# Kernel tuning notes

Hardware: AMD Instinct MI355X
Metric: run time of the kernel (lower is better)

The kernel has to match this reference:

```python
import jax, jax.numpy as jnp
import numpy as np

N = 50000       # nodes
E = 1600000     # edges (before self-loops)
IN = 128        # in_channels
HID = 64        # hidden_channels
HEADS = 2
OUT = 16        # out_channels
NEG_SLOPE = 0.2 # PyG GATConv default leaky_relu slope


def setup_inputs() -> dict:
    key = jax.random.key(0)
    ks = jax.random.split(key, 12)
    g = lambda k, shp, s=0.1: (jax.random.normal(k, shp, dtype=jnp.float32) * s)
    return {
        "x": jax.random.normal(ks[0], (N, IN), dtype=jnp.float32),
        "edge_index": jax.random.randint(ks[1], (2, E), 0, N, dtype=jnp.int32),
        # layer 0: in -> hidden, heads concat
        "W0": g(ks[2], (IN, HEADS * HID)),
        "as0": g(ks[3], (HEADS, HID)),
        "ad0": g(ks[4], (HEADS, HID)),
        "b0": jnp.zeros((HEADS * HID,), jnp.float32),
        # layer 1: hidden*heads -> hidden, heads concat
        "W1": g(ks[5], (HEADS * HID, HEADS * HID)),
        "as1": g(ks[6], (HEADS, HID)),
        "ad1": g(ks[7], (HEADS, HID)),
        "b1": jnp.zeros((HEADS * HID,), jnp.float32),
        # layer 2: hidden*heads -> out, heads averaged (concat=False)
        "W2": g(ks[8], (HEADS * HID, HEADS * OUT)),
        "as2": g(ks[9], (HEADS, OUT)),
        "ad2": g(ks[10], (HEADS, OUT)),
        "b2": jnp.zeros((OUT,), jnp.float32),
    }


def gat_conv(x, src, dst, W, a_src, a_dst, b, concat):
    """PyG-style GATConv (inference; self-loops already in src/dst)."""
    n = x.shape[0]
    H, C = a_src.shape
    h = (x @ W).reshape(n, H, C)                      # [N,H,C]
    alpha_s = jnp.einsum('nhc,hc->nh', h, a_src)      # [N,H]
    alpha_d = jnp.einsum('nhc,hc->nh', h, a_dst)      # [N,H]
    e = alpha_s[src] + alpha_d[dst]                   # [E,H]
    e = jax.nn.leaky_relu(e, NEG_SLOPE)
    # softmax over incoming edges per destination node
    m = jax.ops.segment_max(e, dst, num_segments=n)   # [N,H]
    w = jnp.exp(e - m[dst])                           # [E,H]
    denom = jax.ops.segment_sum(w, dst, num_segments=n)
    alpha = w / (denom[dst] + 1e-16)                  # [E,H]
    out = jax.ops.segment_sum(alpha[:, :, None] * h[src], dst, num_segments=n)  # [N,H,C]
    out = out.reshape(n, H * C) if concat else out.mean(axis=1)
    return out + b


def reference(x, edge_index, W0, as0, ad0, b0, W1, as1, ad1, b1, W2, as2, ad2, b2):
    loop = jnp.arange(N, dtype=edge_index.dtype)
    src = jnp.concatenate([edge_index[0], loop])
    dst = jnp.concatenate([edge_index[1], loop])
    h = jax.nn.elu(gat_conv(x, src, dst, W0, as0, ad0, b0, concat=True))
    h = jax.nn.elu(gat_conv(h, src, dst, W1, as1, ad1, b1, concat=True))
    return gat_conv(h, src, dst, W2, as2, ad2, b2, concat=False)
```

## Files before the change

### kernel.cpp

```cpp
#include <hip/hip_runtime.h>
#include <hip/hip_fp16.h>
#include <cstdint>
#include <cstddef>
#include <type_traits>

constexpr int kN   = 50000;
constexpr int kE   = 1600000;
constexpr int kET  = kE + kN;
constexpr float kNEG = 0.2f;
constexpr int NBUCK = (kN + 127) / 128;
constexpr int CAPB  = 5120;
constexpr int PCHUNK = 4096;
constexpr int PGRID = (kET + PCHUNK - 1) / PCHUNK;

__global__ __launch_bounds__(256) void partition_kernel(const int* __restrict__ ei,
                                                        int* __restrict__ bcnt,
                                                        unsigned* __restrict__ part) {
  __shared__ int hist[NBUCK];
  __shared__ int resv[NBUCK];
  __shared__ int lcnt[NBUCK];
  const int t = threadIdx.x;
  for (int i = t; i < NBUCK; i += 256) hist[i] = 0;
  __syncthreads();
  const int c0 = blockIdx.x * PCHUNK;
  const int cend = (c0 + PCHUNK < kET) ? c0 + PCHUNK : kET;
  for (int i = c0 + t; i < cend; i += 256) {
    const int dst = (i < kE) ? ei[kE + i] : (i - kE);
    atomicAdd(&hist[dst >> 7], 1);
  }
  __syncthreads();
  for (int i = t; i < NBUCK; i += 256) {
    lcnt[i] = 0;
    if (hist[i]) resv[i] = i * CAPB + atomicAdd(&bcnt[i], hist[i]);
  }
  __syncthreads();
  for (int i = c0 + t; i < cend; i += 256) {
    int src, dst;
    if (i < kE) { src = ei[i]; dst = ei[kE + i]; }
    else        { src = i - kE; dst = src; }
    const int b = dst >> 7;
    const int off = atomicAdd(&lcnt[b], 1);
    part[resv[b] + off] = ((unsigned)(dst & 127) << 16) | (unsigned)src;
  }
}

__global__ __launch_bounds__(256) void finalize_kernel(const unsigned* __restrict__ part,
                                                       const int* __restrict__ bcnt,
                                                       int* __restrict__ row_beg,
                                                       int* __restrict__ row_cnt,
                                                       int* __restrict__ col_src) {
  __shared__ int cnt[128];
  __shared__ int sc[128];
  __shared__ int nbase[128];
  const int b = blockIdx.x, t = threadIdx.x;
  const int lo = b * CAPB;
  const int hi = lo + bcnt[b];
  if (t < 128) cnt[t] = 0;
  __syncthreads();
  for (int j = lo + t; j < hi; j += 256) atomicAdd(&cnt[part[j] >> 16], 1);
  __syncthreads();
  if (t < 128) sc[t] = cnt[t];
  __syncthreads();
  for (int off = 1; off < 128; off <<= 1) {
    int v = 0;
    if (t < 128 && t >= off) v = sc[t - off];
    __syncthreads();
    if (t < 128) sc[t] += v;
    __syncthreads();
  }
  if (t < 128) {
    const int c = cnt[t];
    nbase[t] = lo + sc[t] - c;
    const int node = b * 128 + t;
    if (node < kN) { row_beg[node] = nbase[t]; row_cnt[node] = c; }
    cnt[t] = 0;
  }
  __syncthreads();
  for (int j = lo + t; j < hi; j += 256) {
    const unsigned v = part[j];
    const int nl = v >> 16;
    const int pos = nbase[nl] + atomicAdd(&cnt[nl], 1);
    col_src[pos] = (int)(v & 0xffffu);
  }
}

template<int MOUT, int TR, typename TIN>
__global__ __launch_bounds__(256) void transform_kernel(
    const TIN* __restrict__ X, const float* __restrict__ W,
    const float* __restrict__ asf, const float* __restrict__ adf,
    __half* __restrict__ H2, float2* __restrict__ AS, float2* __restrict__ AD, int n) {
  constexpr int CG = MOUT / 4;
  constexpr int RG = 256 / CG;
  constexpr int ROWS = RG * TR;
  __shared__ float Xs[ROWS][132];
  const int t = threadIdx.x;
  const int row0 = blockIdx.x * ROWS;
  if constexpr (std::is_same<TIN, float>::value) {
    for (int i = t; i < ROWS * 32; i += 256) {
      const int r = i >> 5, kc = i & 31;
      float4 v = make_float4(0.f, 0.f, 0.f, 0.f);
      if (row0 + r < n) v = ((const float4*)(X + (size_t)(row0 + r) * 128))[kc];
      *(float4*)(&Xs[r][kc * 4]) = v;
    }
  } else {
    for (int i = t; i < ROWS * 16; i += 256) {
      const int r = i >> 4, kc = i & 15;
      union { uint4 u; __half2 h[4]; } raw;
      raw.u = make_uint4(0u, 0u, 0u, 0u);
      if (row0 + r < n) raw.u = *(const uint4*)(X + (size_t)(row0 + r) * 128 + kc * 8);
      const float2 f0 = __half22float2(raw.h[0]);
      const float2 f1 = __half22float2(raw.h[1]);
      const float2 f2 = __half22float2(raw.h[2]);
      const float2 f3 = __half22float2(raw.h[3]);
      *(float4*)(&Xs[r][kc * 8])     = make_float4(f0.x, f0.y, f1.x, f1.y);
      *(float4*)(&Xs[r][kc * 8 + 4]) = make_float4(f2.x, f2.y, f3.x, f3.y);
    }
  }
  __syncthreads();
  const int cg = t % CG;
  const int rg = t / CG;
  const int c0 = cg * 4;
  float4 acc[TR];
#pragma unroll
  for (int i = 0; i < TR; i++) acc[i] = make_float4(0.f, 0.f, 0.f, 0.f);
  for (int k4 = 0; k4 < 32; k4++) {
    float4 wv0 = *(const float4*)(W + (size_t)(k4 * 4 + 0) * MOUT + c0);
    float4 wv1 = *(const float4*)(W + (size_t)(k4 * 4 + 1) * MOUT + c0);
    float4 wv2 = *(const float4*)(W + (size_t)(k4 * 4 + 2) * MOUT + c0);
    float4 wv3 = *(const float4*)(W + (size_t)(k4 * 4 + 3) * MOUT + c0);
#pragma unroll
    for (int i = 0; i < TR; i++) {
      const float4 xv = *(const float4*)(&Xs[rg * TR + i][k4 * 4]);
      acc[i].x = fmaf(xv.x, wv0.x, acc[i].x); acc[i].y = fmaf(xv.x, wv0.y, acc[i].y);
      acc[i].z = fmaf(xv.x, wv0.z, acc[i].z); acc[i].w = fmaf(xv.x, wv0.w, acc[i].w);
      acc[i].x = fmaf(xv.y, wv1.x, acc[i].x); acc[i].y = fmaf(xv.y, wv1.y, acc[i].y);
      acc[i].z = fmaf(xv.y, wv1.z, acc[i].z); acc[i].w = fmaf(xv.y, wv1.w, acc[i].w);
      acc[i].x = fmaf(xv.z, wv2.x, acc[i].x); acc[i].y = fmaf(xv.z, wv2.y, acc[i].y);
      acc[i].z = fmaf(xv.z, wv2.z, acc[i].z); acc[i].w = fmaf(xv.z, wv2.w, acc[i].w);
      acc[i].x = fmaf(xv.w, wv3.x, acc[i].x); acc[i].y = fmaf(xv.w, wv3.y, acc[i].y);
      acc[i].z = fmaf(xv.w, wv3.z, acc[i].z); acc[i].w = fmaf(xv.w, wv3.w, acc[i].w);
    }
  }
#pragma unroll
  for (int i = 0; i < TR; i++) {
    const int r = row0 + rg * TR + i;
    if (r < n) {
      union { __half2 h[2]; uint2 u; } pk;
      pk.h[0] = __floats2half2_rn(acc[i].x, acc[i].y);
      pk.h[1] = __floats2half2_rn(acc[i].z, acc[i].w);
      *(uint2*)(H2 + (size_t)r * MOUT + c0) = pk.u;
    }
  }
  const float4 av = *(const float4*)(asf + c0);
  const float4 dv = *(const float4*)(adf + c0);
  float sred[TR], dred[TR];
#pragma unroll
  for (int i = 0; i < TR; i++) {
    sred[i] = acc[i].x * av.x + acc[i].y * av.y + acc[i].z * av.z + acc[i].w * av.w;
    dred[i] = acc[i].x * dv.x + acc[i].y * dv.y + acc[i].z * dv.z + acc[i].w * dv.w;
  }
#pragma unroll
  for (int off = 1; off < CG / 2; off <<= 1) {
#pragma unroll
    for (int i = 0; i < TR; i++) {
      sred[i] += __shfl_xor(sred[i], off);
      dred[i] += __shfl_xor(dred[i], off);
    }
  }
  const int lane = t & 63;
#pragma unroll
  for (int i = 0; i < TR; i++) {
    const float s1 = __shfl(sred[i], lane + CG / 2);
    const float d1 = __shfl(dred[i], lane + CG / 2);
    if (cg == 0) {
      const int r = row0 + rg * TR + i;
      if (r < n) { AS[r] = make_float2(sred[i], s1); AD[r] = make_float2(dred[i], d1); }
    }
  }
}

template<int C, int MODE, typename TOUT>
__global__ __launch_bounds__(256) void agg_kernel(
    const __half* __restrict__ H2, const float2* __restrict__ AS,
    const float2* __restrict__ AD, const int* __restrict__ row_beg,
    const int* __restrict__ row_cnt, const int* __restrict__ col_src,
    const float* __restrict__ bias, TOUT* __restrict__ OUT) {
  const int wid  = threadIdx.x >> 6;
  const int lane = threadIdx.x & 63;
  const int node = blockIdx.x * 4 + wid;

  const int begin = row_beg[node];
  const int d = row_cnt[node];
  const float2 adn = AD[node];

  int srcv = 0;
  unsigned pkw = 0;
  float sum0 = 0.f, sum1 = 0.f;
  if (lane < d) {
    srcv = col_src[begin + lane];
    const float2 a = AS[srcv];
    float e0 = a.x + adn.x; e0 = (e0 > 0.f) ? e0 : kNEG * e0;
    float e1 = a.y + adn.y; e1 = (e1 > 0.f) ? e1 : kNEG * e1;
    sum0 = __expf(e0); sum1 = __expf(e1);
    const __half2 ph = __floats2half2_rn(sum0, sum1);
    pkw = *(const unsigned*)&ph;
  }
  for (int j = 64 + lane; j < d; j += 64) {
    const int s = col_src[begin + j];
    const float2 a = AS[s];
    float e0 = a.x + adn.x; e0 = (e0 > 0.f) ? e0 : kNEG * e0;
    float e1 = a.y + adn.y; e1 = (e1 > 0.f) ? e1 : kNEG * e1;
    sum0 += __expf(e0); sum1 += __expf(e1);
  }
#pragma unroll
  for (int off = 32; off >= 1; off >>= 1) {
    sum0 += __shfl_xor(sum0, off);
    sum1 += __shfl_xor(sum1, off);
  }
  const float inv0 = 1.0f / (sum0 + 1e-16f);
  const float inv1 = 1.0f / (sum1 + 1e-16f);

  const int dr = (d < 64) ? d : 64;

  if constexpr (MODE == 0) {
    const int e = lane >> 4;
    const int q = lane & 15;
    const int hsel = (q >= 8);
    const unsigned sel = hsel ? 0x03020302u : 0x01000100u;
    const float inv = hsel ? inv1 : inv0;
    float4 a0 = make_float4(0.f, 0.f, 0.f, 0.f);
    float4 a1 = make_float4(0.f, 0.f, 0.f, 0.f);
    int j = 0;
    while (j < dr) {
      const int jend = (j + 32 < dr) ? j + 32 : dr;
      __half2 hz; *(unsigned*)&hz = 0u;
      __half2 hc0 = hz, hc1 = hz, hc2 = hz, hc3 = hz;
      for (; j < jend; j += 4) {
        const int jj = j + e;
        const int s = __shfl(srcv, jj);
        const unsigned pw = __shfl((int)pkw, jj);
        union { unsigned u; __half2 h; } wv;
        wv.u = __builtin_amdgcn_perm(pw, pw, sel);
        union { uint4 u; __half2 h[4]; } raw;
        raw.u = *(const uint4*)(H2 + (size_t)s * 128 + 8 * q);
        hc0 = __hfma2(wv.h, raw.h[0], hc0);
        hc1 = __hfma2(wv.h, raw.h[1], hc1);
        hc2 = __hfma2(wv.h, raw.h[2], hc2);
        hc3 = __hfma2(wv.h, raw.h[3], hc3);
      }
      float2 f;
      f = __half22float2(hc0); a0.x += f.x; a0.y += f.y;
      f = __half22float2(hc1); a0.z += f.x; a0.w += f.y;
      f = __half22float2(hc2); a1.x += f.x; a1.y += f.y;
      f = __half22float2(hc3); a1.z += f.x; a1.w += f.y;
    }
    for (int jt = 64 + e; jt < d; jt += 4) {
      const int s = col_src[begin + jt];
      const float2 a = AS[s];
      float e0 = a.x + adn.x; e0 = (e0 > 0.f) ? e0 : kNEG * e0;
      float e1 = a.y + adn.y; e1 = (e1 > 0.f) ? e1 : kNEG * e1;
      const float w = hsel ? __expf(e1) : __expf(e0);
      union { uint4 u; __half2 h[4]; } raw;
      raw.u = *(const uint4*)(H2 + (size_t)s * 128 + 8 * q);
      const float2 f0 = __half22float2(raw.h[0]);
      const float2 f1 = __half22float2(raw.h[1]);
      const float2 f2 = __half22float2(raw.h[2]);
      const float2 f3 = __half22float2(raw.h[3]);
      a0.x = fmaf(w, f0.x, a0.x); a0.y = fmaf(w, f0.y, a0.y);
      a0.z = fmaf(w, f1.x, a0.z); a0.w = fmaf(w, f1.y, a0.w);
      a1.x = fmaf(w, f2.x, a1.x); a1.y = fmaf(w, f2.y, a1.y);
      a1.z = fmaf(w, f3.x, a1.z); a1.w = fmaf(w, f3.y, a1.w);
    }
#pragma unroll
    for (int off = 32; off >= 16; off >>= 1) {
      a0.x += __shfl_xor(a0.x, off); a0.y += __shfl_xor(a0.y, off);
      a0.z += __shfl_xor(a0.z, off); a0.w += __shfl_xor(a0.w, off);
      a1.x += __shfl_xor(a1.x, off); a1.y += __shfl_xor(a1.y, off);
      a1.z += __shfl_xor(a1.z, off); a1.w += __shfl_xor(a1.w, off);
    }
    if (lane < 16) {
      const int ch = 8 * q;
      const float4 b0v = *(const float4*)(bias + ch);
      const float4 b1v = *(const float4*)(bias + ch + 4);
      float4 o0, o1;
      o0.x = a0.x * inv + b0v.x; o0.y = a0.y * inv + b0v.y;
      o0.z = a0.z * inv + b0v.z; o0.w = a0.w * inv + b0v.w;
      o1.x = a1.x * inv + b1v.x; o1.y = a1.y * inv + b1v.y;
      o1.z = a1.z * inv + b1v.z; o1.w = a1.w * inv + b1v.w;
      o0.x = (o0.x > 0.f) ? o0.x : expm1f(o0.x);
      o0.y = (o0.y > 0.f) ? o0.y : expm1f(o0.y);
      o0.z = (o0.z > 0.f) ? o0.z : expm1f(o0.z);
      o0.w = (o0.w > 0.f) ? o0.w : expm1f(o0.w);
      o1.x = (o1.x > 0.f) ? o1.x : expm1f(o1.x);
      o1.y = (o1.y > 0.f) ? o1.y : expm1f(o1.y);
      o1.z = (o1.z > 0.f) ? o1.z : expm1f(o1.z);
      o1.w = (o1.w > 0.f) ? o1.w : expm1f(o1.w);
      if constexpr (std::is_same<TOUT, __half>::value) {
        union { __half2 h[4]; uint4 u; } pk;
        pk.h[0] = __floats2half2_rn(o0.x, o0.y);
        pk.h[1] = __floats2half2_rn(o0.z, o0.w);
        pk.h[2] = __floats2half2_rn(o1.x, o1.y);
        pk.h[3] = __floats2half2_rn(o1.z, o1.w);
        *(uint4*)(OUT + (size_t)node * 128 + ch) = pk.u;
      } else {
        *(float4*)((float*)OUT + (size_t)node * 128 + ch) = o0;
        *(float4*)((float*)OUT + (size_t)node * 128 + ch + 4) = o1;
      }
    }
  } else {
    const int e = lane >> 3;
    const int q = lane & 7;
    const int hsel = (q >= 4);
    const unsigned sel = hsel ? 0x03020302u : 0x01000100u;
    const float inv = hsel ? inv1 : inv0;
    __half2 hz; *(unsigned*)&hz = 0u;
    __half2 hc0 = hz, hc1 = hz;
    for (int j = 0; j < dr; j += 8) {
      const int jj = j + e;
      const int s = __shfl(srcv, jj);
      const unsigned pw = __shfl((int)pkw, jj);
      union { unsigned u; __half2 h; } wv;
      wv.u = __builtin_amdgcn_perm(pw, pw, sel);
      union { uint2 u; __half2 h[2]; } raw;
      raw.u = *(const uint2*)(H2 + (size_t)s * 32 + 4 * q);
      hc0 = __hfma2(wv.h, raw.h[0], hc0);
      hc1 = __hfma2(wv.h, raw.h[1], hc1);
    }
    float4 acc;
    float2 f;
    f = __half22float2(hc0); acc.x = f.x; acc.y = f.y;
    f = __half22float2(hc1); acc.z = f.x; acc.w = f.y;
    for (int jt = 64 + e; jt < d; jt += 8) {
      const int s = col_src[begin + jt];
      const float2 a = AS[s];
      float e0 = a.x + adn.x; e0 = (e0 > 0.f) ? e0 : kNEG * e0;
      float e1 = a.y + adn.y; e1 = (e1 > 0.f) ? e1 : kNEG * e1;
      const float w = hsel ? __expf(e1) : __expf(e0);
      union { uint2 u; __half2 h[2]; } raw;
      raw.u = *(const uint2*)(H2 + (size_t)s * 32 + 4 * q);
      const float2 f0 = __half22float2(raw.h[0]);
      const float2 f1 = __half22float2(raw.h[1]);
      acc.x = fmaf(w, f0.x, acc.x); acc.y = fmaf(w, f0.y, acc.y);
      acc.z = fmaf(w, f1.x, acc.z); acc.w = fmaf(w, f1.y, acc.w);
    }
#pragma unroll
    for (int off = 32; off >= 8; off >>= 1) {
      acc.x += __shfl_xor(acc.x, off); acc.y += __shfl_xor(acc.y, off);
      acc.z += __shfl_xor(acc.z, off); acc.w += __shfl_xor(acc.w, off);
    }
    acc.x *= inv; acc.y *= inv; acc.z *= inv; acc.w *= inv;
    const float px = __shfl_xor(acc.x, 4);
    const float py = __shfl_xor(acc.y, 4);
    const float pz = __shfl_xor(acc.z, 4);
    const float pw = __shfl_xor(acc.w, 4);
    if (lane < 4) {
      const int ch = 4 * q;
      const float4 bv = *(const float4*)(bias + ch);
      float4 o;
      o.x = 0.5f * (acc.x + px) + bv.x;
      o.y = 0.5f * (acc.y + py) + bv.y;
      o.z = 0.5f * (acc.z + pz) + bv.z;
      o.w = 0.5f * (acc.w + pw) + bv.w;
      *(float4*)((float*)OUT + (size_t)node * 16 + ch) = o;
    }
  }
}

extern "C" void kernel_launch(void* const* d_in, const int* in_sizes, int n_in,
                              void* d_out, int out_size, void* d_ws, size_t ws_size,
                              hipStream_t stream) {
  const float* x   = (const float*)d_in[0];
  const int*   ei  = (const int*)d_in[1];
  const float* W0  = (const float*)d_in[2];
  const float* as0 = (const float*)d_in[3];
  const float* ad0 = (const float*)d_in[4];
  const float* b0  = (const float*)d_in[5];
  const float* W1  = (const float*)d_in[6];
  const float* as1 = (const float*)d_in[7];
  const float* ad1 = (const float*)d_in[8];
  const float* b1  = (const float*)d_in[9];
  const float* W2  = (const float*)d_in[10];
  const float* as2 = (const float*)d_in[11];
  const float* ad2 = (const float*)d_in[12];
  const float* b2  = (const float*)d_in[13];
  float* out = (float*)d_out;

  size_t off = 0;
  auto alloc = [&](size_t bytes) -> void* {
    void* p = (char*)d_ws + off;
    off += (bytes + 255) & ~(size_t)255;
    return p;
  };
  int*    row_beg = (int*)alloc(sizeof(int) * kN);
  int*    row_cnt = (int*)alloc(sizeof(int) * kN);
  int*    bcnt    = (int*)alloc(sizeof(int) * NBUCK);
  int*    col_src = (int*)alloc(sizeof(int) * (size_t)NBUCK * CAPB);
  float2* AS      = (float2*)alloc(sizeof(float2) * kN);
  float2* AD      = (float2*)alloc(sizeof(float2) * kN);
  __half* H2      = (__half*)alloc(sizeof(__half) * (size_t)kN * 128);
  __half* actA    = (__half*)alloc(sizeof(__half) * (size_t)kN * 128);
  __half* actB    = (__half*)alloc(sizeof(__half) * (size_t)kN * 128);
  unsigned* part  = (unsigned*)actA;
  (void)ws_size; (void)in_sizes; (void)n_in; (void)out_size;

  hipMemsetAsync(bcnt, 0, sizeof(int) * NBUCK, stream);
  partition_kernel<<<PGRID, 256, 0, stream>>>(ei, bcnt, part);
  finalize_kernel<<<NBUCK, 256, 0, stream>>>(part, bcnt, row_beg, row_cnt, col_src);

  transform_kernel<128, 4, float><<<(kN + 31) / 32, 256, 0, stream>>>(x, W0, as0, ad0, H2, AS, AD, kN);
  agg_kernel<64, 0, __half><<<(kN + 3) / 4, 256, 0, stream>>>(H2, AS, AD, row_beg, row_cnt, col_src, b0, actA);

  transform_kernel<128, 4, __half><<<(kN + 31) / 32, 256, 0, stream>>>(actA, W1, as1, ad1, H2, AS, AD, kN);
  agg_kernel<64, 0, __half><<<(kN + 3) / 4, 256, 0, stream>>>(H2, AS, AD, row_beg, row_cnt, col_src, b1, actB);

  transform_kernel<32, 1, __half><<<(kN + 31) / 32, 256, 0, stream>>>(actB, W2, as2, ad2, H2, AS, AD, kN);
  agg_kernel<16, 1, float><<<(kN + 3) / 4, 256, 0, stream>>>(H2, AS, AD, row_beg, row_cnt, col_src, b2, out);
}
```

Measured before the change: 300.7 us.

## Split attention weights into separate pass and quarter-partition aggregation by channel

```diff
diff --git a/kernel.cpp b/kernel.cpp
--- a/kernel.cpp
+++ b/kernel.cpp
@@ -12,6 +12,7 @@
 constexpr int CAPB  = 5120;
 constexpr int PCHUNK = 4096;
 constexpr int PGRID = (kET + PCHUNK - 1) / PCHUNK;
+constexpr int QSTRIDE = kN * 32;
 
 __global__ __launch_bounds__(256) void partition_kernel(const int* __restrict__ ei,
                                                         int* __restrict__ bcnt,
@@ -148,7 +149,13 @@
       union { __half2 h[2]; uint2 u; } pk;
       pk.h[0] = __floats2half2_rn(acc[i].x, acc[i].y);
       pk.h[1] = __floats2half2_rn(acc[i].z, acc[i].w);
-      *(uint2*)(H2 + (size_t)r * MOUT + c0) = pk.u;
+      if constexpr (MOUT == 128) {
+        const int qq = cg >> 3;
+        const int co = (cg & 7) * 4;
+        *(uint2*)(H2 + (size_t)qq * QSTRIDE + (size_t)r * 32 + co) = pk.u;
+      } else {
+        *(uint2*)(H2 + (size_t)r * MOUT + c0) = pk.u;
+      }
     }
   }
   const float4 av = *(const float4*)(asf + c0);
@@ -179,32 +186,28 @@
   }
 }
 
-template<int C, int MODE, typename TOUT>
-__global__ __launch_bounds__(256) void agg_kernel(
-    const __half* __restrict__ H2, const float2* __restrict__ AS,
-    const float2* __restrict__ AD, const int* __restrict__ row_beg,
-    const int* __restrict__ row_cnt, const int* __restrict__ col_src,
-    const float* __restrict__ bias, TOUT* __restrict__ OUT) {
+__global__ __launch_bounds__(256) void weight_kernel(
+    const float2* __restrict__ AS, const float2* __restrict__ AD,
+    const int* __restrict__ row_beg, const int* __restrict__ row_cnt,
+    const int* __restrict__ col_src,
+    unsigned* __restrict__ rec0, unsigned* __restrict__ rec1) {
   const int wid  = threadIdx.x >> 6;
   const int lane = threadIdx.x & 63;
   const int node = blockIdx.x * 4 + wid;
-
   const int begin = row_beg[node];
   const int d = row_cnt[node];
   const float2 adn = AD[node];
 
   int srcv = 0;
-  unsigned pkw = 0;
-  float sum0 = 0.f, sum1 = 0.f;
+  float w0 = 0.f, w1 = 0.f;
   if (lane < d) {
     srcv = col_src[begin + lane];
     const float2 a = AS[srcv];
     float e0 = a.x + adn.x; e0 = (e0 > 0.f) ? e0 : kNEG * e0;
     float e1 = a.y + adn.y; e1 = (e1 > 0.f) ? e1 : kNEG * e1;
-    sum0 = __expf(e0); sum1 = __expf(e1);
-    const __half2 ph = __floats2half2_rn(sum0, sum1);
-    pkw = *(const unsigned*)&ph;
-  }
+    w0 = __expf(e0); w1 = __expf(e1);
+  }
+  float sum0 = w0, sum1 = w1;
   for (int j = 64 + lane; j < d; j += 64) {
     const int s = col_src[begin + j];
     const float2 a = AS[s];
@@ -219,150 +222,154 @@
   }
   const float inv0 = 1.0f / (sum0 + 1e-16f);
   const float inv1 = 1.0f / (sum1 + 1e-16f);
-
-  const int dr = (d < 64) ? d : 64;
-
-  if constexpr (MODE == 0) {
-    const int e = lane >> 4;
-    const int q = lane & 15;
-    const int hsel = (q >= 8);
-    const unsigned sel = hsel ? 0x03020302u : 0x01000100u;
-    const float inv = hsel ? inv1 : inv0;
-    float4 a0 = make_float4(0.f, 0.f, 0.f, 0.f);
-    float4 a1 = make_float4(0.f, 0.f, 0.f, 0.f);
-    int j = 0;
-    while (j < dr) {
-      const int jend = (j + 32 < dr) ? j + 32 : dr;
-      __half2 hz; *(unsigned*)&hz = 0u;
-      __half2 hc0 = hz, hc1 = hz, hc2 = hz, hc3 = hz;
-      for (; j < jend; j += 4) {
-        const int jj = j + e;
-        const int s = __shfl(srcv, jj);
-        const unsigned pw = __shfl((int)pkw, jj);
-        union { unsigned u; __half2 h; } wv;
-        wv.u = __builtin_amdgcn_perm(pw, pw, sel);
-        union { uint4 u; __half2 h[4]; } raw;
-        raw.u = *(const uint4*)(H2 + (size_t)s * 128 + 8 * q);
-        hc0 = __hfma2(wv.h, raw.h[0], hc0);
-        hc1 = __hfma2(wv.h, raw.h[1], hc1);
-        hc2 = __hfma2(wv.h, raw.h[2], hc2);
-        hc3 = __hfma2(wv.h, raw.h[3], hc3);
-      }
-      float2 f;
-      f = __half22float2(hc0); a0.x += f.x; a0.y += f.y;
-      f = __half22float2(hc1); a0.z += f.x; a0.w += f.y;
-      f = __half22float2(hc2); a1.x += f.x; a1.y += f.y;
-      f = __half22float2(hc3); a1.z += f.x; a1.w += f.y;
-    }
-    for (int jt = 64 + e; jt < d; jt += 4) {
-      const int s = col_src[begin + jt];
-      const float2 a = AS[s];
-      float e0 = a.x + adn.x; e0 = (e0 > 0.f) ? e0 : kNEG * e0;
-      float e1 = a.y + adn.y; e1 = (e1 > 0.f) ? e1 : kNEG * e1;
-      const float w = hsel ? __expf(e1) : __expf(e0);
+  if (lane < d) {
+    const unsigned h0 = (unsigned)__half_as_ushort(__float2half_rn(w0 * inv0));
+    const unsigned h1 = (unsigned)__half_as_ushort(__float2half_rn(w1 * inv1));
+    rec0[begin + lane] = (unsigned)srcv | (h0 << 16);
+    rec1[begin + lane] = (unsigned)srcv | (h1 << 16);
+  }
+  for (int j = 64 + lane; j < d; j += 64) {
+    const int s = col_src[begin + j];
+    const float2 a = AS[s];
+    float e0 = a.x + adn.x; e0 = (e0 > 0.f) ? e0 : kNEG * e0;
+    float e1 = a.y + adn.y; e1 = (e1 > 0.f) ? e1 : kNEG * e1;
+    const unsigned h0 = (unsigned)__half_as_ushort(__float2half_rn(__expf(e0) * inv0));
+    const unsigned h1 = (unsigned)__half_as_ushort(__float2half_rn(__expf(e1) * inv1));
+    rec0[begin + j] = (unsigned)s | (h0 << 16);
+    rec1[begin + j] = (unsigned)s | (h1 << 16);
+  }
+}
+
+__global__ __launch_bounds__(256) void agg64q_kernel(
+    const __half* __restrict__ H2q, const unsigned* __restrict__ rec0,
+    const unsigned* __restrict__ rec1, const int* __restrict__ row_beg,
+    const int* __restrict__ row_cnt, const float* __restrict__ bias,
+    __half* __restrict__ OUT) {
+  const int bid = blockIdx.x;
+  const int qtr = (bid & 7) >> 1;
+  const int ng  = ((bid >> 3) << 1) | (bid & 1);
+  const int wid  = threadIdx.x >> 6;
+  const int lane = threadIdx.x & 63;
+  const int node = ng * 4 + wid;
+  const int begin = row_beg[node];
+  const int d = row_cnt[node];
+  const unsigned* __restrict__ rec = (qtr >= 2) ? rec1 : rec0;
+  const int strm = lane >> 2;
+  const int cq   = lane & 3;
+  const __half* __restrict__ Hq = H2q + (size_t)qtr * QSTRIDE;
+
+  float4 f0 = make_float4(0.f, 0.f, 0.f, 0.f);
+  float4 f1 = make_float4(0.f, 0.f, 0.f, 0.f);
+  int j = 0;
+  while (j < d) {
+    const int jend = (j + 64 < d) ? j + 64 : d;
+    __half2 hz; *(unsigned*)&hz = 0u;
+    __half2 hc0 = hz, hc1 = hz, hc2 = hz, hc3 = hz;
+    for (; j < jend; j += 16) {
+      const int jo = j + strm;
+      const int jc = (jo < d) ? jo : 0;
+      unsigned r = rec[begin + jc];
+      if (jo >= d) r &= 0xffffu;
+      union { unsigned u; __half2 h; } wv;
+      wv.u = __builtin_amdgcn_perm(r, r, 0x03020302u);
       union { uint4 u; __half2 h[4]; } raw;
-      raw.u = *(const uint4*)(H2 + (size_t)s * 128 + 8 * q);
-      const float2 f0 = __half22float2(raw.h[0]);
-      const float2 f1 = __half22float2(raw.h[1]);
-      const float2 f2 = __half22float2(raw.h[2]);
-      const float2 f3 = __half22float2(raw.h[3]);
-      a0.x = fmaf(w, f0.x, a0.x); a0.y = fmaf(w, f0.y, a0.y);
-      a0.z = fmaf(w, f1.x, a0.z); a0.w = fmaf(w, f1.y, a0.w);
-      a1.x = fmaf(w, f2.x, a1.x); a1.y = fmaf(w, f2.y, a1.y);
-      a1.z = fmaf(w, f3.x, a1.z); a1.w = fmaf(w, f3.y, a1.w);
-    }
-#pragma unroll
-    for (int off = 32; off >= 16; off >>= 1) {
-      a0.x += __shfl_xor(a0.x, off); a0.y += __shfl_xor(a0.y, off);
-      a0.z += __shfl_xor(a0.z, off); a0.w += __shfl_xor(a0.w, off);
-      a1.x += __shfl_xor(a1.x, off); a1.y += __shfl_xor(a1.y, off);
-      a1.z += __shfl_xor(a1.z, off); a1.w += __shfl_xor(a1.w, off);
-    }
-    if (lane < 16) {
-      const int ch = 8 * q;
-      const float4 b0v = *(const float4*)(bias + ch);
-      const float4 b1v = *(const float4*)(bias + ch + 4);
-      float4 o0, o1;
-      o0.x = a0.x * inv + b0v.x; o0.y = a0.y * inv + b0v.y;
-      o0.z = a0.z * inv + b0v.z; o0.w = a0.w * inv + b0v.w;
-      o1.x = a1.x * inv + b1v.x; o1.y = a1.y * inv + b1v.y;
-      o1.z = a1.z * inv + b1v.z; o1.w = a1.w * inv + b1v.w;
-      o0.x = (o0.x > 0.f) ? o0.x : expm1f(o0.x);
-      o0.y = (o0.y > 0.f) ? o0.y : expm1f(o0.y);
-      o0.z = (o0.z > 0.f) ? o0.z : expm1f(o0.z);
-      o0.w = (o0.w > 0.f) ? o0.w : expm1f(o0.w);
-      o1.x = (o1.x > 0.f) ? o1.x : expm1f(o1.x);
-      o1.y = (o1.y > 0.f) ? o1.y : expm1f(o1.y);
-      o1.z = (o1.z > 0.f) ? o1.z : expm1f(o1.z);
-      o1.w = (o1.w > 0.f) ? o1.w : expm1f(o1.w);
-      if constexpr (std::is_same<TOUT, __half>::value) {
-        union { __half2 h[4]; uint4 u; } pk;
-        pk.h[0] = __floats2half2_rn(o0.x, o0.y);
-        pk.h[1] = __floats2half2_rn(o0.z, o0.w);
-        pk.h[2] = __floats2half2_rn(o1.x, o1.y);
-        pk.h[3] = __floats2half2_rn(o1.z, o1.w);
-        *(uint4*)(OUT + (size_t)node * 128 + ch) = pk.u;
-      } else {
-        *(float4*)((float*)OUT + (size_t)node * 128 + ch) = o0;
-        *(float4*)((float*)OUT + (size_t)node * 128 + ch + 4) = o1;
-      }
-    }
-  } else {
-    const int e = lane >> 3;
-    const int q = lane & 7;
-    const int hsel = (q >= 4);
-    const unsigned sel = hsel ? 0x03020302u : 0x01000100u;
-    const float inv = hsel ? inv1 : inv0;
+      raw.u = *(const uint4*)(Hq + (size_t)(r & 0xffffu) * 32 + (cq << 3));
+      hc0 = __hfma2(wv.h, raw.h[0], hc0);
+      hc1 = __hfma2(wv.h, raw.h[1], hc1);
+      hc2 = __hfma2(wv.h, raw.h[2], hc2);
+      hc3 = __hfma2(wv.h, raw.h[3], hc3);
+    }
+    float2 f;
+    f = __half22float2(hc0); f0.x += f.x; f0.y += f.y;
+    f = __half22float2(hc1); f0.z += f.x; f0.w += f.y;
+    f = __half22float2(hc2); f1.x += f.x; f1.y += f.y;
+    f = __half22float2(hc3); f1.z += f.x; f1.w += f.y;
+  }
+#pragma unroll
+  for (int off = 32; off >= 4; off >>= 1) {
+    f0.x += __shfl_xor(f0.x, off); f0.y += __shfl_xor(f0.y, off);
+    f0.z += __shfl_xor(f0.z, off); f0.w += __shfl_xor(f0.w, off);
+    f1.x += __shfl_xor(f1.x, off); f1.y += __shfl_xor(f1.y, off);
+    f1.z += __shfl_xor(f1.z, off); f1.w += __shfl_xor(f1.w, off);
+  }
+  if (lane < 4) {
+    const int ch = qtr * 32 + lane * 8;
+    const float4 b0v = *(const float4*)(bias + ch);
+    const float4 b1v = *(const float4*)(bias + ch + 4);
+    float4 o0, o1;
+    o0.x = f0.x + b0v.x; o0.y = f0.y + b0v.y; o0.z = f0.z + b0v.z; o0.w = f0.w + b0v.w;
+    o1.x = f1.x + b1v.x; o1.y = f1.y + b1v.y; o1.z = f1.z + b1v.z; o1.w = f1.w + b1v.w;
+    o0.x = (o0.x > 0.f) ? o0.x : expm1f(o0.x);
+    o0.y = (o0.y > 0.f) ? o0.y : expm1f(o0.y);
+    o0.z = (o0.z > 0.f) ? o0.z : expm1f(o0.z);
+    o0.w = (o0.w > 0.f) ? o0.w : expm1f(o0.w);
+    o1.x = (o1.x > 0.f) ? o1.x : expm1f(o1.x);
+    o1.y = (o1.y > 0.f) ? o1.y : expm1f(o1.y);
+    o1.z = (o1.z > 0.f) ? o1.z : expm1f(o1.z);
+    o1.w = (o1.w > 0.f) ? o1.w : expm1f(o1.w);
+    union { __half2 h[4]; uint4 u; } pk;
+    pk.h[0] = __floats2half2_rn(o0.x, o0.y);
+    pk.h[1] = __floats2half2_rn(o0.z, o0.w);
+    pk.h[2] = __floats2half2_rn(o1.x, o1.y);
+    pk.h[3] = __floats2half2_rn(o1.z, o1.w);
+    *(uint4*)(OUT + (size_t)node * 128 + ch) = pk.u;
+  }
+}
+
+__global__ __launch_bounds__(256) void agg16r_kernel(
+    const __half* __restrict__ H2, const unsigned* __restrict__ rec0,
+    const unsigned* __restrict__ rec1, const int* __restrict__ row_beg,
+    const int* __restrict__ row_cnt, const float* __restrict__ bias,
+    float* __restrict__ OUT) {
+  const int wid  = threadIdx.x >> 6;
+  const int lane = threadIdx.x & 63;
+  const int node = blockIdx.x * 4 + wid;
+  const int begin = row_beg[node];
+  const int d = row_cnt[node];
+  const int strm = lane >> 3;
+  const int q    = lane & 7;
+  const unsigned* __restrict__ rec = (q >= 4) ? rec1 : rec0;
+
+  float4 acc = make_float4(0.f, 0.f, 0.f, 0.f);
+  int j = 0;
+  while (j < d) {
+    const int jend = (j + 64 < d) ? j + 64 : d;
     __half2 hz; *(unsigned*)&hz = 0u;
     __half2 hc0 = hz, hc1 = hz;
-    for (int j = 0; j < dr; j += 8) {
-      const int jj = j + e;
-      const int s = __shfl(srcv, jj);
-      const unsigned pw = __shfl((int)pkw, jj);
+    for (; j < jend; j += 8) {
+      const int jo = j + strm;
+      const int jc = (jo < d) ? jo : 0;
+      unsigned r = rec[begin + jc];
+      if (jo >= d) r &= 0xffffu;
       union { unsigned u; __half2 h; } wv;
-      wv.u = __builtin_amdgcn_perm(pw, pw, sel);
+      wv.u = __builtin_amdgcn_perm(r, r, 0x03020302u);
       union { uint2 u; __half2 h[2]; } raw;
-      raw.u = *(const uint2*)(H2 + (size_t)s * 32 + 4 * q);
+      raw.u = *(const uint2*)(H2 + (size_t)(r & 0xffffu) * 32 + (q << 2));
       hc0 = __hfma2(wv.h, raw.h[0], hc0);
       hc1 = __hfma2(wv.h, raw.h[1], hc1);
     }
-    float4 acc;
     float2 f;
-    f = __half22float2(hc0); acc.x = f.x; acc.y = f.y;
-    f = __half22float2(hc1); acc.z = f.x; acc.w = f.y;
-    for (int jt = 64 + e; jt < d; jt += 8) {
-      const int s = col_src[begin + jt];
-      const float2 a = AS[s];
-      float e0 = a.x + adn.x; e0 = (e0 > 0.f) ? e0 : kNEG * e0;
-      float e1 = a.y + adn.y; e1 = (e1 > 0.f) ? e1 : kNEG * e1;
-      const float w = hsel ? __expf(e1) : __expf(e0);
-      union { uint2 u; __half2 h[2]; } raw;
-      raw.u = *(const uint2*)(H2 + (size_t)s * 32 + 4 * q);
-      const float2 f0 = __half22float2(raw.h[0]);
-      const float2 f1 = __half22float2(raw.h[1]);
-      acc.x = fmaf(w, f0.x, acc.x); acc.y = fmaf(w, f0.y, acc.y);
-      acc.z = fmaf(w, f1.x, acc.z); acc.w = fmaf(w, f1.y, acc.w);
-    }
-#pragma unroll
-    for (int off = 32; off >= 8; off >>= 1) {
-      acc.x += __shfl_xor(acc.x, off); acc.y += __shfl_xor(acc.y, off);
-      acc.z += __shfl_xor(acc.z, off); acc.w += __shfl_xor(acc.w, off);
-    }
-    acc.x *= inv; acc.y *= inv; acc.z *= inv; acc.w *= inv;
-    const float px = __shfl_xor(acc.x, 4);
-    const float py = __shfl_xor(acc.y, 4);
-    const float pz = __shfl_xor(acc.z, 4);
-    const float pw = __shfl_xor(acc.w, 4);
-    if (lane < 4) {
-      const int ch = 4 * q;
-      const float4 bv = *(const float4*)(bias + ch);
-      float4 o;
-      o.x = 0.5f * (acc.x + px) + bv.x;
-      o.y = 0.5f * (acc.y + py) + bv.y;
-      o.z = 0.5f * (acc.z + pz) + bv.z;
-      o.w = 0.5f * (acc.w + pw) + bv.w;
-      *(float4*)((float*)OUT + (size_t)node * 16 + ch) = o;
-    }
+    f = __half22float2(hc0); acc.x += f.x; acc.y += f.y;
+    f = __half22float2(hc1); acc.z += f.x; acc.w += f.y;
+  }
+#pragma unroll
+  for (int off = 32; off >= 8; off >>= 1) {
+    acc.x += __shfl_xor(acc.x, off); acc.y += __shfl_xor(acc.y, off);
+    acc.z += __shfl_xor(acc.z, off); acc.w += __shfl_xor(acc.w, off);
+  }
+  const float px = __shfl_xor(acc.x, 4);
+  const float py = __shfl_xor(acc.y, 4);
+  const float pz = __shfl_xor(acc.z, 4);
+  const float pw = __shfl_xor(acc.w, 4);
+  if (lane < 4) {
+    const int ch = 4 * q;
+    const float4 bv = *(const float4*)(bias + ch);
+    float4 o;
+    o.x = 0.5f * (acc.x + px) + bv.x;
+    o.y = 0.5f * (acc.y + py) + bv.y;
+    o.z = 0.5f * (acc.z + pz) + bv.z;
+    o.w = 0.5f * (acc.w + pw) + bv.w;
+    *(float4*)(OUT + (size_t)node * 16 + ch) = o;
   }
 }
 
@@ -391,28 +398,35 @@
     off += (bytes + 255) & ~(size_t)255;
     return p;
   };
-  int*    row_beg = (int*)alloc(sizeof(int) * kN);
-  int*    row_cnt = (int*)alloc(sizeof(int) * kN);
-  int*    bcnt    = (int*)alloc(sizeof(int) * NBUCK);
-  int*    col_src = (int*)alloc(sizeof(int) * (size_t)NBUCK * CAPB);
-  float2* AS      = (float2*)alloc(sizeof(float2) * kN);
-  float2* AD      = (float2*)alloc(sizeof(float2) * kN);
-  __half* H2      = (__half*)alloc(sizeof(__half) * (size_t)kN * 128);
-  __half* actA    = (__half*)alloc(sizeof(__half) * (size_t)kN * 128);
-  __half* actB    = (__half*)alloc(sizeof(__half) * (size_t)kN * 128);
-  unsigned* part  = (unsigned*)actA;
+  int*      row_beg = (int*)alloc(sizeof(int) * kN);
+  int*      row_cnt = (int*)alloc(sizeof(int) * kN);
+  int*      bcnt    = (int*)alloc(sizeof(int) * NBUCK);
+  int*      col_src = (int*)alloc(sizeof(int) * (size_t)NBUCK * CAPB);
+  unsigned* rec0    = (unsigned*)alloc(sizeof(unsigned) * (size_t)NBUCK * CAPB);
+  unsigned* rec1    = (unsigned*)alloc(sizeof(unsigned) * (size_t)NBUCK * CAPB);
+  float2*   AS      = (float2*)alloc(sizeof(float2) * kN);
+  float2*   AD      = (float2*)alloc(sizeof(float2) * kN);
+  __half*   H2      = (__half*)alloc(sizeof(__half) * (size_t)kN * 128);
+  __half*   actA    = (__half*)alloc(sizeof(__half) * (size_t)kN * 128);
+  __half*   actB    = (__half*)alloc(sizeof(__half) * (size_t)kN * 128);
+  unsigned* part    = (unsigned*)actA;
   (void)ws_size; (void)in_sizes; (void)n_in; (void)out_size;
 
   hipMemsetAsync(bcnt, 0, sizeof(int) * NBUCK, stream);
   partition_kernel<<<PGRID, 256, 0, stream>>>(ei, bcnt, part);
   finalize_kernel<<<NBUCK, 256, 0, stream>>>(part, bcnt, row_beg, row_cnt, col_src);
 
+  const int ngrid = kN / 4;
+
   transform_kernel<128, 4, float><<<(kN + 31) / 32, 256, 0, stream>>>(x, W0, as0, ad0, H2, AS, AD, kN);
-  agg_kernel<64, 0, __half><<<(kN + 3) / 4, 256, 0, stream>>>(H2, AS, AD, row_beg, row_cnt, col_src, b0, actA);
+  weight_kernel<<<ngrid, 256, 0, stream>>>(AS, AD, row_beg, row_cnt, col_src, rec0, rec1);
+  agg64q_kernel<<<kN, 256, 0, stream>>>(H2, rec0, rec1, row_beg, row_cnt, b0, actA);
 
   transform_kernel<128, 4, __half><<<(kN + 31) / 32, 256, 0, stream>>>(actA, W1, as1, ad1, H2, AS, AD, kN);
-  agg_kernel<64, 0, __half><<<(kN + 3) / 4, 256, 0, stream>>>(H2, AS, AD, row_beg, row_cnt, col_src, b1, actB);
+  weight_kernel<<<ngrid, 256, 0, stream>>>(AS, AD, row_beg, row_cnt, col_src, rec0, rec1);
+  agg64q_kernel<<<kN, 256, 0, stream>>>(H2, rec0, rec1, row_beg, row_cnt, b1, actB);
 
   transform_kernel<32, 1, __half><<<(kN + 31) / 32, 256, 0, stream>>>(actB, W2, as2, ad2, H2, AS, AD, kN);
-  agg_kernel<16, 1, float><<<(kN + 3) / 4, 256, 0, stream>>>(H2, AS, AD, row_beg, row_cnt, col_src, b2, out);
-}
+  weight_kernel<<<ngrid, 256, 0, stream>>>(AS, AD, row_beg, row_cnt, col_src, rec0, rec1);
+  agg16r_kernel<<<ngrid, 256, 0, stream>>>(H2, rec0, rec1, row_beg, row_cnt, b2, out);
+}
```

Result: slower. 427.2 us (+42.0%).

## Replace scalar FMA dense transforms with MFMA fp16 matrix-core kernels

Applied to the files above, without the earlier changes.

```diff
diff --git a/kernel.cpp b/kernel.cpp
--- a/kernel.cpp
+++ b/kernel.cpp
@@ -12,6 +12,9 @@
 constexpr int CAPB  = 5120;
 constexpr int PCHUNK = 4096;
 constexpr int PGRID = (kET + PCHUNK - 1) / PCHUNK;
+
+typedef _Float16 f16x8 __attribute__((ext_vector_type(8)));
+typedef float    f32x4 __attribute__((ext_vector_type(4)));
 
 __global__ __launch_bounds__(256) void partition_kernel(const int* __restrict__ ei,
                                                         int* __restrict__ bcnt,
@@ -84,98 +87,88 @@
   }
 }
 
-template<int MOUT, int TR, typename TIN>
-__global__ __launch_bounds__(256) void transform_kernel(
-    const TIN* __restrict__ X, const float* __restrict__ W,
+__global__ __launch_bounds__(256) void prep_w_kernel(
+    const float* __restrict__ W0, const float* __restrict__ W1,
+    const float* __restrict__ W2, __half* __restrict__ Wt0,
+    __half* __restrict__ Wt1, __half* __restrict__ Wt2) {
+  int i = blockIdx.x * 256 + threadIdx.x;
+  const int stride = gridDim.x * 256;
+  for (; i < 16384 * 2 + 4096; i += stride) {
+    if (i < 16384) {
+      const int k = i >> 7, c = i & 127;
+      Wt0[c * 128 + k] = __float2half_rn(W0[i]);
+    } else if (i < 32768) {
+      const int j = i - 16384, k = j >> 7, c = j & 127;
+      Wt1[c * 128 + k] = __float2half_rn(W1[j]);
+    } else {
+      const int j = i - 32768, k = j >> 5, c = j & 31;
+      Wt2[c * 128 + k] = __float2half_rn(W2[j]);
+    }
+  }
+}
+
+template<int NCOL, typename TIN>
+__global__ __launch_bounds__(256) void mfma_transform_kernel(
+    const TIN* __restrict__ X, const __half* __restrict__ Wt,
     const float* __restrict__ asf, const float* __restrict__ adf,
     __half* __restrict__ H2, float2* __restrict__ AS, float2* __restrict__ AD, int n) {
-  constexpr int CG = MOUT / 4;
-  constexpr int RG = 256 / CG;
-  constexpr int ROWS = RG * TR;
-  __shared__ float Xs[ROWS][132];
-  const int t = threadIdx.x;
-  const int row0 = blockIdx.x * ROWS;
-  if constexpr (std::is_same<TIN, float>::value) {
-    for (int i = t; i < ROWS * 32; i += 256) {
-      const int r = i >> 5, kc = i & 31;
-      float4 v = make_float4(0.f, 0.f, 0.f, 0.f);
-      if (row0 + r < n) v = ((const float4*)(X + (size_t)(row0 + r) * 128))[kc];
-      *(float4*)(&Xs[r][kc * 4]) = v;
-    }
-  } else {
-    for (int i = t; i < ROWS * 16; i += 256) {
-      const int r = i >> 4, kc = i & 15;
-      union { uint4 u; __half2 h[4]; } raw;
-      raw.u = make_uint4(0u, 0u, 0u, 0u);
-      if (row0 + r < n) raw.u = *(const uint4*)(X + (size_t)(row0 + r) * 128 + kc * 8);
-      const float2 f0 = __half22float2(raw.h[0]);
-      const float2 f1 = __half22float2(raw.h[1]);
-      const float2 f2 = __half22float2(raw.h[2]);
-      const float2 f3 = __half22float2(raw.h[3]);
-      *(float4*)(&Xs[r][kc * 8])     = make_float4(f0.x, f0.y, f1.x, f1.y);
-      *(float4*)(&Xs[r][kc * 8 + 4]) = make_float4(f2.x, f2.y, f3.x, f3.y);
-    }
-  }
-  __syncthreads();
-  const int cg = t % CG;
-  const int rg = t / CG;
-  const int c0 = cg * 4;
-  float4 acc[TR];
-#pragma unroll
-  for (int i = 0; i < TR; i++) acc[i] = make_float4(0.f, 0.f, 0.f, 0.f);
-  for (int k4 = 0; k4 < 32; k4++) {
-    float4 wv0 = *(const float4*)(W + (size_t)(k4 * 4 + 0) * MOUT + c0);
-    float4 wv1 = *(const float4*)(W + (size_t)(k4 * 4 + 1) * MOUT + c0);
-    float4 wv2 = *(const float4*)(W + (size_t)(k4 * 4 + 2) * MOUT + c0);
-    float4 wv3 = *(const float4*)(W + (size_t)(k4 * 4 + 3) * MOUT + c0);
-#pragma unroll
-    for (int i = 0; i < TR; i++) {
-      const float4 xv = *(const float4*)(&Xs[rg * TR + i][k4 * 4]);
-      acc[i].x = fmaf(xv.x, wv0.x, acc[i].x); acc[i].y = fmaf(xv.x, wv0.y, acc[i].y);
-      acc[i].z = fmaf(xv.x, wv0.z, acc[i].z); acc[i].w = fmaf(xv.x, wv0.w, acc[i].w);
-      acc[i].x = fmaf(xv.y, wv1.x, acc[i].x); acc[i].y = fmaf(xv.y, wv1.y, acc[i].y);
-      acc[i].z = fmaf(xv.y, wv1.z, acc[i].z); acc[i].w = fmaf(xv.y, wv1.w, acc[i].w);
-      acc[i].x = fmaf(xv.z, wv2.x, acc[i].x); acc[i].y = fmaf(xv.z, wv2.y, acc[i].y);
-      acc[i].z = fmaf(xv.z, wv2.z, acc[i].z); acc[i].w = fmaf(xv.z, wv2.w, acc[i].w);
-      acc[i].x = fmaf(xv.w, wv3.x, acc[i].x); acc[i].y = fmaf(xv.w, wv3.y, acc[i].y);
-      acc[i].z = fmaf(xv.w, wv3.z, acc[i].z); acc[i].w = fmaf(xv.w, wv3.w, acc[i].w);
-    }
-  }
-#pragma unroll
-  for (int i = 0; i < TR; i++) {
-    const int r = row0 + rg * TR + i;
-    if (r < n) {
-      union { __half2 h[2]; uint2 u; } pk;
-      pk.h[0] = __floats2half2_rn(acc[i].x, acc[i].y);
-      pk.h[1] = __floats2half2_rn(acc[i].z, acc[i].w);
-      *(uint2*)(H2 + (size_t)r * MOUT + c0) = pk.u;
-    }
-  }
-  const float4 av = *(const float4*)(asf + c0);
-  const float4 dv = *(const float4*)(adf + c0);
-  float sred[TR], dred[TR];
-#pragma unroll
-  for (int i = 0; i < TR; i++) {
-    sred[i] = acc[i].x * av.x + acc[i].y * av.y + acc[i].z * av.z + acc[i].w * av.w;
-    dred[i] = acc[i].x * dv.x + acc[i].y * dv.y + acc[i].z * dv.z + acc[i].w * dv.w;
-  }
-#pragma unroll
-  for (int off = 1; off < CG / 2; off <<= 1) {
-#pragma unroll
-    for (int i = 0; i < TR; i++) {
-      sred[i] += __shfl_xor(sred[i], off);
-      dred[i] += __shfl_xor(dred[i], off);
-    }
-  }
-  const int lane = t & 63;
-#pragma unroll
-  for (int i = 0; i < TR; i++) {
-    const float s1 = __shfl(sred[i], lane + CG / 2);
-    const float d1 = __shfl(dred[i], lane + CG / 2);
-    if (cg == 0) {
-      const int r = row0 + rg * TR + i;
-      if (r < n) { AS[r] = make_float2(sred[i], s1); AD[r] = make_float2(dred[i], d1); }
-    }
+  constexpr int NT = NCOL / 16;
+  const int wid  = threadIdx.x >> 6;
+  const int lane = threadIdx.x & 63;
+  const int rbase = blockIdx.x * 64 + wid * 16;
+  if (rbase >= n) return;
+  const int r  = rbase + (lane & 15);
+  const int kg = (lane >> 4) * 8;
+  const _Float16* __restrict__ Wf = (const _Float16*)Wt;
+
+  f32x4 acc[NT];
+#pragma unroll
+  for (int t = 0; t < NT; t++) acc[t] = (f32x4){0.f, 0.f, 0.f, 0.f};
+
+#pragma unroll
+  for (int kc = 0; kc < 4; kc++) {
+    const int kh = kc * 32 + kg;
+    f16x8 bfrag;
+    if constexpr (std::is_same<TIN, float>::value) {
+      const float4 v0 = *(const float4*)(X + (size_t)r * 128 + kh);
+      const float4 v1 = *(const float4*)(X + (size_t)r * 128 + kh + 4);
+      bfrag[0] = (_Float16)v0.x; bfrag[1] = (_Float16)v0.y;
+      bfrag[2] = (_Float16)v0.z; bfrag[3] = (_Float16)v0.w;
+      bfrag[4] = (_Float16)v1.x; bfrag[5] = (_Float16)v1.y;
+      bfrag[6] = (_Float16)v1.z; bfrag[7] = (_Float16)v1.w;
+    } else {
+      bfrag = *(const f16x8*)((const _Float16*)X + (size_t)r * 128 + kh);
+    }
+#pragma unroll
+    for (int t = 0; t < NT; t++) {
+      const f16x8 afrag = *(const f16x8*)(Wf + (size_t)(t * 16 + (lane & 15)) * 128 + kh);
+      acc[t] = __builtin_amdgcn_mfma_f32_16x16x32_f16(afrag, bfrag, acc[t], 0, 0, 0);
+    }
+  }
+
+  const int c4 = (lane >> 4) * 4;
+  float s0 = 0.f, s1 = 0.f, d0 = 0.f, d1 = 0.f;
+#pragma unroll
+  for (int t = 0; t < NT; t++) {
+    const int c0 = t * 16 + c4;
+    const float4 av = *(const float4*)(asf + c0);
+    const float4 dv = *(const float4*)(adf + c0);
+    const float ps = acc[t][0] * av.x + acc[t][1] * av.y + acc[t][2] * av.z + acc[t][3] * av.w;
+    const float pd = acc[t][0] * dv.x + acc[t][1] * dv.y + acc[t][2] * dv.z + acc[t][3] * dv.w;
+    if (t < NT / 2) { s0 += ps; d0 += pd; } else { s1 += ps; d1 += pd; }
+    union { __half2 h[2]; uint2 u; } pk;
+    pk.h[0] = __floats2half2_rn(acc[t][0], acc[t][1]);
+    pk.h[1] = __floats2half2_rn(acc[t][2], acc[t][3]);
+    *(uint2*)(H2 + (size_t)r * NCOL + c0) = pk.u;
+  }
+#pragma unroll
+  for (int off = 16; off <= 32; off <<= 1) {
+    s0 += __shfl_xor(s0, off); s1 += __shfl_xor(s1, off);
+    d0 += __shfl_xor(d0, off); d1 += __shfl_xor(d1, off);
+  }
+  if (lane < 16) {
+    AS[rbase + lane] = make_float2(s0, s1);
+    AD[rbase + lane] = make_float2(d0, d1);
   }
 }
 
@@ -295,17 +288,12 @@
       o1.y = (o1.y > 0.f) ? o1.y : expm1f(o1.y);
       o1.z = (o1.z > 0.f) ? o1.z : expm1f(o1.z);
       o1.w = (o1.w > 0.f) ? o1.w : expm1f(o1.w);
-      if constexpr (std::is_same<TOUT, __half>::value) {
-        union { __half2 h[4]; uint4 u; } pk;
-        pk.h[0] = __floats2half2_rn(o0.x, o0.y);
-        pk.h[1] = __floats2half2_rn(o0.z, o0.w);
-        pk.h[2] = __floats2half2_rn(o1.x, o1.y);
-        pk.h[3] = __floats2half2_rn(o1.z, o1.w);
-        *(uint4*)(OUT + (size_t)node * 128 + ch) = pk.u;
-      } else {
-        *(float4*)((float*)OUT + (size_t)node * 128 + ch) = o0;
-        *(float4*)((float*)OUT + (size_t)node * 128 + ch + 4) = o1;
-      }
+      union { __half2 h[4]; uint4 u; } pk;
+      pk.h[0] = __floats2half2_rn(o0.x, o0.y);
+      pk.h[1] = __floats2half2_rn(o0.z, o0.w);
+      pk.h[2] = __floats2half2_rn(o1.x, o1.y);
+      pk.h[3] = __floats2half2_rn(o1.z, o1.w);
+      *(uint4*)((__half*)OUT + (size_t)node * 128 + ch) = pk.u;
     }
   } else {
     const int e = lane >> 3;
@@ -352,7 +340,7 @@
     const float px = __shfl_xor(acc.x, 4);
     const float py = __shfl_xor(acc.y, 4);
     const float pz = __shfl_xor(acc.z, 4);
-    const float pw = __shfl_xor(acc.w, 4);
+    const float pw2 = __shfl_xor(acc.w, 4);
     if (lane < 4) {
       const int ch = 4 * q;
       const float4 bv = *(const float4*)(bias + ch);
@@ -360,7 +348,7 @@
       o.x = 0.5f * (acc.x + px) + bv.x;
       o.y = 0.5f * (acc.y + py) + bv.y;
       o.z = 0.5f * (acc.z + pz) + bv.z;
-      o.w = 0.5f * (acc.w + pw) + bv.w;
+      o.w = 0.5f * (acc.w + pw2) + bv.w;
       *(float4*)((float*)OUT + (size_t)node * 16 + ch) = o;
     }
   }
@@ -400,19 +388,26 @@
   __half* H2      = (__half*)alloc(sizeof(__half) * (size_t)kN * 128);
   __half* actA    = (__half*)alloc(sizeof(__half) * (size_t)kN * 128);
   __half* actB    = (__half*)alloc(sizeof(__half) * (size_t)kN * 128);
+  __half* Wt0     = (__half*)alloc(sizeof(__half) * 128 * 128);
+  __half* Wt1     = (__half*)alloc(sizeof(__half) * 128 * 128);
+  __half* Wt2     = (__half*)alloc(sizeof(__half) * 32 * 128);
   unsigned* part  = (unsigned*)actA;
   (void)ws_size; (void)in_sizes; (void)n_in; (void)out_size;
 
   hipMemsetAsync(bcnt, 0, sizeof(int) * NBUCK, stream);
+  prep_w_kernel<<<144, 256, 0, stream>>>(W0, W1, W2, Wt0, Wt1, Wt2);
   partition_kernel<<<PGRID, 256, 0, stream>>>(ei, bcnt, part);
   finalize_kernel<<<NBUCK, 256, 0, stream>>>(part, bcnt, row_beg, row_cnt, col_src);
 
-  transform_kernel<128, 4, float><<<(kN + 31) / 32, 256, 0, stream>>>(x, W0, as0, ad0, H2, AS, AD, kN);
-  agg_kernel<64, 0, __half><<<(kN + 3) / 4, 256, 0, stream>>>(H2, AS, AD, row_beg, row_cnt, col_src, b0, actA);
-
-  transform_kernel<128, 4, __half><<<(kN + 31) / 32, 256, 0, stream>>>(actA, W1, as1, ad1, H2, AS, AD, kN);
-  agg_kernel<64, 0, __half><<<(kN + 3) / 4, 256, 0, stream>>>(H2, AS, AD, row_beg, row_cnt, col_src, b1, actB);
-
-  transform_kernel<32, 1, __half><<<(kN + 31) / 32, 256, 0, stream>>>(actB, W2, as2, ad2, H2, AS, AD, kN);
-  agg_kernel<16, 1, float><<<(kN + 3) / 4, 256, 0, stream>>>(H2, AS, AD, row_beg, row_cnt, col_src, b2, out);
-}
+  const int tgrid = (kN + 63) / 64;
+  const int ngrid = kN / 4;
+
+  mfma_transform_kernel<128, float><<<tgrid, 256, 0, stream>>>(x, Wt0, as0, ad0, H2, AS, AD, kN);
+  agg_kernel<64, 0, __half><<<ngrid, 256, 0, stream>>>(H2, AS, AD, row_beg, row_cnt, col_src, b0, actA);
+
+  mfma_transform_kernel<128, __half><<<tgrid, 256, 0, stream>>>(actA, Wt1, as1, ad1, H2, AS, AD, kN);
+  agg_kernel<64, 0, __half><<<ngrid, 256, 0, stream>>>(H2, AS, AD, row_beg, row_cnt, col_src, b1, actB);
+
+  mfma_transform_kernel<32, __half><<<tgrid, 256, 0, stream>>>(actB, Wt2, as2, ad2, H2, AS, AD, kN);
+  agg_kernel<16, 1, float><<<ngrid, 256, 0, stream>>>(H2, AS, AD, row_beg, row_cnt, col_src, b2, out);
+}
```

Measured after the change: 263.0 us. 12.6% less time.
